# Kernel tuning notes

Hardware: AMD Instinct MI355X
Metric: run time of the kernel (lower is better)

Reference implementation:

```python
import jax, jax.numpy as jnp
import numpy as np

B, T, DIM, H = 2, 2048, 2048, 16
HD = DIM // H  # 128
ROPE_BASE = 10000.0


def _rope_angles(seq_len, head_dim, offset=0, dtype=jnp.float32):
    inv_freq = 1.0 / (ROPE_BASE ** (jnp.arange(0, head_dim, 2, dtype=dtype) / head_dim))
    pos = jnp.arange(offset, offset + seq_len, dtype=dtype)
    ang = pos[:, None] * inv_freq[None, :]              # [T, HD/2]
    ang = jnp.concatenate([ang, ang], axis=-1)          # [T, HD]
    return jnp.cos(ang), jnp.sin(ang)


def _rotate_half(x):
    x1, x2 = jnp.split(x, 2, axis=-1)
    return jnp.concatenate([-x2, x1], axis=-1)


def setup_inputs() -> dict:
    key = jax.random.key(0)
    ks = jax.random.split(key, 5)
    s = 0.02
    return {
        "x": jax.random.normal(ks[0], (B, T, DIM), dtype=jnp.float32),
        "Wq": jax.random.normal(ks[1], (DIM, DIM), dtype=jnp.float32) * s,
        "Wk": jax.random.normal(ks[2], (DIM, HD), dtype=jnp.float32) * s,
        "Wv": jax.random.normal(ks[3], (DIM, HD), dtype=jnp.float32) * s,
        "Wo": jax.random.normal(ks[4], (DIM, DIM), dtype=jnp.float32) * s,
    }


def reference(x, Wq, Wk, Wv, Wo):
    # q: [B, H, T, HD]; k, v: single shared head [B, T, HD]
    q = (x @ Wq).reshape(B, T, H, HD).transpose(0, 2, 1, 3)
    k = x @ Wk
    v = x @ Wv

    # RoPE (offset=0, no kv cache)
    cos, sin = _rope_angles(T, HD, 0, x.dtype)
    q = q * cos[None, None] + _rotate_half(q) * sin[None, None]
    k = k * cos[None] + _rotate_half(k) * sin[None]

    present_k = k[:, None]  # [B, 1, T, HD]
    present_v = v[:, None]

    # MQA attention: broadcast shared KV head via einsum (no materialized expand)
    scale = 1.0 / jnp.sqrt(jnp.asarray(HD, x.dtype))
    scores = jnp.einsum('bhqd,bkd->bhqk', q, k) * scale  # [B, H, T, T]
    causal = jnp.tril(jnp.ones((T, T), dtype=bool))
    scores = jnp.where(causal[None, None], scores, jnp.finfo(scores.dtype).min)
    attn = jax.nn.softmax(scores, axis=-1)
    out = jnp.einsum('bhqk,bkd->bhqd', attn, v)          # [B, H, T, HD]
    out = out.transpose(0, 2, 1, 3).reshape(B, T, DIM) @ Wo
    return (out, present_k, present_v)
```

## Files before the change

### kernel.cpp

```cpp
#include <hip/hip_runtime.h>


typedef __attribute__((ext_vector_type(8))) short short8;
typedef __attribute__((ext_vector_type(4))) float float4v;
typedef __attribute__((ext_vector_type(4))) unsigned short ushort4v;

#define LOG2E 1.4426950408889634f
#define ATT_SCALE 0.08838834764831845f
#define RLOG 0.20762050593046014f

__device__ __forceinline__ float bf2f(ushort u) {
    union { unsigned u; float f; } v; v.u = ((unsigned)u) << 16; return v.f;
}
__device__ __forceinline__ ushort f2bf(float f) {
    union { float f; unsigned u; } v; v.f = f;
    return (ushort)((v.u + 0x7FFF + ((v.u >> 16) & 1)) >> 16);
}
__device__ __forceinline__ ushort f2bf_fast(float f) {
    union { float f; unsigned u; } v; v.f = f;
    return (ushort)((v.u + 0x8000u) >> 16);
}
__device__ __forceinline__ float4v mfma16(short8 a, short8 b, float4v c) {
    return __builtin_amdgcn_mfma_f32_16x16x32_bf16(a, b, c, 0, 0, 0);
}
__device__ __forceinline__ void gl_lds16(const ushort* g, ushort* l) {
    __builtin_amdgcn_global_load_lds(
        (const __attribute__((address_space(1))) unsigned int*)g,
        (__attribute__((address_space(3))) unsigned int*)l, 16, 0, 0);
}

__global__ __launch_bounds__(256) void prep(const float* __restrict__ x,
                                            ushort* __restrict__ x_bf,
                                            float* __restrict__ tbl) {
    int bid = blockIdx.x;
    if (bid < 512) {
        int idx = bid * 256 + threadIdx.x;
        int d = idx & 63, t = idx >> 6;
        float inv = exp2f(-(float)d * RLOG);
        float s, c;
        sincosf((float)t * inv, &s, &c);
        tbl[idx * 2] = c;  tbl[idx * 2 + 1] = s;
    } else {
        int i = ((bid - 512) * 256 + threadIdx.x) * 4;
        float4v v = *(const float4v*)&x[i];
        ushort4v u;
        #pragma unroll
        for (int r = 0; r < 4; ++r) u[r] = f2bf(v[r]);
        *(ushort4v*)&x_bf[i] = u;
    }
}

__global__ __launch_bounds__(256) void transpose_cvt(const float* __restrict__ in,
                                                     ushort* __restrict__ out,
                                                     int M, int N) {
    __shared__ ushort tile[32][33];
    int cb = blockIdx.x * 32, rb = blockIdx.y * 32;
    int x = threadIdx.x, y0 = threadIdx.y;
    #pragma unroll
    for (int i = 0; i < 32; i += 8)
        tile[y0 + i][x] = f2bf(in[(long)(rb + y0 + i) * N + cb + x]);
    __syncthreads();
    #pragma unroll
    for (int i = 0; i < 32; i += 8)
        out[(long)(cb + y0 + i) * M + rb + x] = tile[x][y0 + i];
}

__global__ __launch_bounds__(256) void transpose_bf16(const ushort* __restrict__ in,
                                                      ushort* __restrict__ out,
                                                      int M, int N) {
    __shared__ ushort tile[32][33];
    int cb = blockIdx.x * 32, rb = blockIdx.y * 32;
    int x = threadIdx.x, y0 = threadIdx.y;
    #pragma unroll
    for (int i = 0; i < 32; i += 8)
        tile[y0 + i][x] = in[(long)(rb + y0 + i) * N + cb + x];
    __syncthreads();
    #pragma unroll
    for (int i = 0; i < 32; i += 8)
        out[(long)(cb + y0 + i) * M + rb + x] = tile[x][y0 + i];
}

__global__ __launch_bounds__(256) void gemm_qkv(const ushort* __restrict__ A,
                                                const ushort* __restrict__ W,
                                                ushort* __restrict__ Cq,
                                                ushort* __restrict__ Ck,
                                                ushort* __restrict__ Cv) {
    constexpr int BM = 128, BN = 128, K = 2048;
    constexpr int SM = 64, SN = 64, MT = 4, NT = 4;
    __shared__ ushort As[BM * 32];
    __shared__ ushort Bs[BN * 32];
    const int m0 = blockIdx.y * BM, n0 = blockIdx.x * BN;
    const int tid = threadIdx.x;
    const int wave = tid >> 6, lane = tid & 63, l15 = lane & 15, quad = lane >> 4;
    const int wr = wave >> 1, wc = wave & 1;

    float4v acc[MT][NT] = {};

    for (int k0 = 0; k0 < K; k0 += 32) {
        __syncthreads();
        #pragma unroll
        for (int p = 0; p < 2; ++p) {
            int lin = (p * 4 + wave) * 64 + lane;
            int row = lin >> 2, c8 = (lin & 3) * 8;
            gl_lds16(&A[(long)(m0 + row) * K + k0 + c8], &As[(p * 4 + wave) * 512]);
        }
        #pragma unroll
        for (int p = 0; p < 2; ++p) {
            int lin = (p * 4 + wave) * 64 + lane;
            int row = lin >> 2, c8 = (lin & 3) * 8;
            gl_lds16(&W[(long)(n0 + row) * K + k0 + c8], &Bs[(p * 4 + wave) * 512]);
        }
        __syncthreads();

        short8 a[MT], b[NT];
        #pragma unroll
        for (int mt = 0; mt < MT; ++mt)
            a[mt] = *(const short8*)&As[(wr * SM + mt * 16 + l15) * 32 + quad * 8];
        #pragma unroll
        for (int nt = 0; nt < NT; ++nt)
            b[nt] = *(const short8*)&Bs[(wc * SN + nt * 16 + l15) * 32 + quad * 8];
        #pragma unroll
        for (int mt = 0; mt < MT; ++mt)
            #pragma unroll
            for (int nt = 0; nt < NT; ++nt)
                acc[mt][nt] = mfma16(a[mt], b[nt], acc[mt][nt]);
    }
    ushort* C;  int Nc, coff;
    if (n0 < 2048)      { C = Cq; Nc = 2048; coff = n0; }
    else if (n0 < 2176) { C = Ck; Nc = 128;  coff = n0 - 2048; }
    else                { C = Cv; Nc = 128;  coff = n0 - 2176; }
    #pragma unroll
    for (int mt = 0; mt < MT; ++mt)
        #pragma unroll
        for (int nt = 0; nt < NT; ++nt)
            #pragma unroll
            for (int r = 0; r < 4; ++r) {
                int row = m0 + wr * SM + mt * 16 + quad * 4 + r;
                int col = coff + wc * SN + nt * 16 + l15;
                C[(long)row * Nc + col] = f2bf(acc[mt][nt][r]);
            }
}

__global__ __launch_bounds__(256) void gemm_out(const ushort* __restrict__ A,
                                                const ushort* __restrict__ W,
                                                float* __restrict__ C) {
    constexpr int BM = 128, BN = 128, K = 2048, N = 2048;
    constexpr int SM = 64, SN = 64, MT = 4, NT = 4;
    __shared__ ushort As[BM * 32];
    __shared__ ushort Bs[BN * 32];
    const int m0 = blockIdx.y * BM, n0 = blockIdx.x * BN;
    const int tid = threadIdx.x;
    const int wave = tid >> 6, lane = tid & 63, l15 = lane & 15, quad = lane >> 4;
    const int wr = wave >> 1, wc = wave & 1;

    float4v acc[MT][NT] = {};

    for (int k0 = 0; k0 < K; k0 += 32) {
        __syncthreads();
        #pragma unroll
        for (int p = 0; p < 2; ++p) {
            int lin = (p * 4 + wave) * 64 + lane;
            int row = lin >> 2, c8 = (lin & 3) * 8;
            gl_lds16(&A[(long)(m0 + row) * K + k0 + c8], &As[(p * 4 + wave) * 512]);
        }
        #pragma unroll
        for (int p = 0; p < 2; ++p) {
            int lin = (p * 4 + wave) * 64 + lane;
            int row = lin >> 2, c8 = (lin & 3) * 8;
            gl_lds16(&W[(long)(n0 + row) * K + k0 + c8], &Bs[(p * 4 + wave) * 512]);
        }
        __syncthreads();

        short8 a[MT], b[NT];
        #pragma unroll
        for (int mt = 0; mt < MT; ++mt)
            a[mt] = *(const short8*)&As[(wr * SM + mt * 16 + l15) * 32 + quad * 8];
        #pragma unroll
        for (int nt = 0; nt < NT; ++nt)
            b[nt] = *(const short8*)&Bs[(wc * SN + nt * 16 + l15) * 32 + quad * 8];
        #pragma unroll
        for (int mt = 0; mt < MT; ++mt)
            #pragma unroll
            for (int nt = 0; nt < NT; ++nt)
                acc[mt][nt] = mfma16(a[mt], b[nt], acc[mt][nt]);
    }
    #pragma unroll
    for (int mt = 0; mt < MT; ++mt)
        #pragma unroll
        for (int nt = 0; nt < NT; ++nt)
            #pragma unroll
            for (int r = 0; r < 4; ++r) {
                int row = m0 + wr * SM + mt * 16 + quad * 4 + r;
                int col = n0 + wc * SN + nt * 16 + l15;
                C[(long)row * N + col] = acc[mt][nt][r];
            }
}

template<int BM, int BN>
__global__ __launch_bounds__(256) void gemm_bt_f32(const float* __restrict__ A32,
                                                   const ushort* __restrict__ B0,
                                                   const ushort* __restrict__ B1,
                                                   ushort* __restrict__ C0,
                                                   ushort* __restrict__ C1,
                                                   int M, int N, int K) {
    constexpr int SM = BM / 2, SN = BN / 2;
    constexpr int MT = SM / 16, NT = SN / 16;
    constexpr int LDK = 40;
    __shared__ ushort As[BM * LDK];
    __shared__ ushort Bs[BN * LDK];
    const ushort* Bm = blockIdx.z ? B1 : B0;
    ushort* C = blockIdx.z ? C1 : C0;
    const int m0 = blockIdx.y * BM, n0 = blockIdx.x * BN;
    const int tid = threadIdx.x;
    const int wave = tid >> 6, lane = tid & 63, l15 = lane & 15, quad = lane >> 4;
    const int wr = wave >> 1, wc = wave & 1;
    float4v acc[MT][NT] = {};
    for (int k0 = 0; k0 < K; k0 += 32) {
        #pragma unroll
        for (int p = 0; p < (BM * 32) / (256 * 4); ++p) {
            int lin = p * 256 + tid;
            int row = lin >> 3, c4 = (lin & 7) * 4;
            float4v v = *(const float4v*)&A32[(long)(m0 + row) * K + k0 + c4];
            ushort4v u;
            #pragma unroll
            for (int i = 0; i < 4; ++i) u[i] = f2bf(v[i]);
            *(ushort4v*)&As[row * LDK + c4] = u;
        }
        #pragma unroll
        for (int p = 0; p < (BN * 4) / 256; ++p) {
            int lin = p * 256 + tid;
            int row = lin >> 2, c8 = (lin & 3) * 8;
            *(short8*)&Bs[row * LDK + c8] =
                *(const short8*)&Bm[(long)(n0 + row) * K + k0 + c8];
        }
        __syncthreads();
        short8 a[MT], b[NT];
        #pragma unroll
        for (int mt = 0; mt < MT; ++mt)
            a[mt] = *(const short8*)&As[(wr * SM + mt * 16 + l15) * LDK + quad * 8];
        #pragma unroll
        for (int nt = 0; nt < NT; ++nt)
            b[nt] = *(const short8*)&Bs[(wc * SN + nt * 16 + l15) * LDK + quad * 8];
        #pragma unroll
        for (int mt = 0; mt < MT; ++mt)
            #pragma unroll
            for (int nt = 0; nt < NT; ++nt)
                acc[mt][nt] = mfma16(a[mt], b[nt], acc[mt][nt]);
        __syncthreads();
    }
    #pragma unroll
    for (int mt = 0; mt < MT; ++mt)
        #pragma unroll
        for (int nt = 0; nt < NT; ++nt)
            #pragma unroll
            for (int r = 0; r < 4; ++r) {
                int row = m0 + wr * SM + mt * 16 + quad * 4 + r;
                int col = n0 + wc * SN + nt * 16 + l15;
                C[(long)row * N + col] = f2bf(acc[mt][nt][r]);
            }
}

__global__ __launch_bounds__(256) void rope_k_present(ushort* __restrict__ Kw,
                                                      const ushort* __restrict__ Vw,
                                                      const float* __restrict__ tbl,
                                                      float* __restrict__ outK,
                                                      float* __restrict__ outV) {
    int idx = blockIdx.x * 256 + threadIdx.x;
    int d = idx & 63;
    int row = idx >> 6;
    int t = row & 2047;
    float c = tbl[(t * 64 + d) * 2], s = tbl[(t * 64 + d) * 2 + 1];
    long base = (long)row * 128 + d;
    float k1 = bf2f(Kw[base]), k2 = bf2f(Kw[base + 64]);
    float r1 = k1 * c - k2 * s, r2 = k2 * c + k1 * s;
    Kw[base] = f2bf(r1);  Kw[base + 64] = f2bf(r2);
    outK[base] = r1;      outK[base + 64] = r2;
    outV[base] = bf2f(Vw[base]); outV[base + 64] = bf2f(Vw[base + 64]);
}

__global__ __launch_bounds__(256, 2) void flash_mqa6(ushort* __restrict__ Q,
                                                     const ushort* __restrict__ Kg,
                                                     const ushort* __restrict__ Vt,
                                                     const float* __restrict__ tbl) {
    constexpr int T = 2048, DIM = 2048;
    constexpr float SCL2 = ATT_SCALE * LOG2E;
    constexpr int LDP = 72;
    __shared__ ushort Ks[2][64 * 128];
    __shared__ ushort Vs[2][128 * 64];
    __shared__ ushort Ps[4][16 * LDP];

    const int j = blockIdx.x;
    const int b = j >> 8, r0 = j & 255;
    const int h = r0 & 15, q4 = r0 >> 4;

    const int tid = threadIdx.x;
    const int wave = tid >> 6, lane = tid & 63, l15 = lane & 15, quad = lane >> 4;
    const int swz = l15 & 7;

    const ushort* kb_ptr = Kg + (long)b * T * 128;
    const ushort* vb_ptr = Vt + (long)b * T;

    auto stage = [&](int buf, int t) {
        const int k0 = t * 64;
        #pragma unroll
        for (int p = 0; p < 4; ++p) {
            int ci = (wave * 4 + p) * 64 + lane;
            int kr = ci >> 4, kc = ci & 15;
            gl_lds16(&kb_ptr[(long)(k0 + kr) * 128 + ((kc ^ (kr & 7)) * 8)],
                     &Ks[buf][(wave * 4 + p) * 512]);
            int vd = ci >> 3, vc = ci & 7;
            gl_lds16(&vb_ptr[(long)vd * 4096 + k0 + ((vc ^ (vd & 7)) * 8)],
                     &Vs[buf][(wave * 4 + p) * 512]);
        }
    };

    #pragma unroll 1
    for (int ht = 0; ht < 2; ++ht) {
        const int qb = ht ? (31 - q4) : q4;
        const int qbase = qb * 64;
        const int tq = qbase + wave * 16 + l15;
        const int nkb = qb + 1;

        short8 qf[4];
        const ushort* qp = Q + (long)(b * T + tq) * DIM + h * 128 + quad * 8;
        #pragma unroll
        for (int kc = 0; kc < 4; ++kc) qf[kc] = *(const short8*)(qp + kc * 32);
        #pragma unroll
        for (int kc = 0; kc < 2; ++kc) {
            float ang[16];
            const float4v* tb = (const float4v*)(tbl + ((long)tq * 64 + kc * 32 + quad * 8) * 2);
            *(float4v*)&ang[0]  = tb[0];
            *(float4v*)&ang[4]  = tb[1];
            *(float4v*)&ang[8]  = tb[2];
            *(float4v*)&ang[12] = tb[3];
            #pragma unroll
            for (int jj = 0; jj < 8; ++jj) {
                float cs = ang[2 * jj] * SCL2, sn = ang[2 * jj + 1] * SCL2;
                float x1 = bf2f((ushort)qf[kc][jj]);
                float x2 = bf2f((ushort)qf[kc + 2][jj]);
                qf[kc][jj]     = (short)f2bf(x1 * cs - x2 * sn);
                qf[kc + 2][jj] = (short)f2bf(x2 * cs + x1 * sn);
            }
        }

        float4v o[8] = {};
        float l_part = 0.f;

        stage(0, 0);
        __syncthreads();

        for (int t = 0; t < nkb; ++t) {
            const int cur = t & 1;
            if (t + 1 < nkb) stage(cur ^ 1, t + 1);

            const ushort* ksb = &Ks[cur][0];
            const ushort* vsb = &Vs[cur][0];

            float4v st[4] = {};
            #pragma unroll
            for (int sub = 0; sub < 4; ++sub) {
                const int r = sub * 16 + l15;
                #pragma unroll
                for (int kc = 0; kc < 4; ++kc) {
                    short8 kf = *(const short8*)&ksb[r * 128 + (((kc * 4 + quad) ^ swz) * 8)];
                    st[sub] = mfma16(kf, qf[kc], st[sub]);
                }
            }

            const int k0 = t * 64;
            const bool diag = (t == nkb - 1);
            ushort* Pw = &Ps[wave][0];
            #pragma unroll
            for (int sub = 0; sub < 4; ++sub) {
                ushort4v pv4;
                #pragma unroll
                for (int rr = 0; rr < 4; ++rr) {
                    float zz = st[sub][rr];
                    if (diag) {
                        int key = k0 + sub * 16 + quad * 4 + rr;
                        zz = (key <= tq) ? zz : -INFINITY;
                    }
                    float pv = exp2f(zz);
                    l_part += pv;
                    pv4[rr] = f2bf_fast(pv);
                }
                *(ushort4v*)&Pw[l15 * LDP + sub * 16 + quad * 4] = pv4;
            }

            #pragma unroll
            for (int hf = 0; hf < 2; ++hf) {
                short8 pf = *(const short8*)&Pw[l15 * LDP + hf * 32 + quad * 8];
                #pragma unroll
                for (int nt = 0; nt < 8; ++nt) {
                    short8 vf = *(const short8*)&vsb[(nt * 16 + l15) * 64 + (((hf * 4 + quad) ^ swz) * 8)];
                    o[nt] = mfma16(vf, pf, o[nt]);
                }
            }
            __syncthreads();
        }

        float rs = l_part;
        rs += __shfl_xor(rs, 16);
        rs += __shfl_xor(rs, 32);
        float inv_l = 1.0f / rs;
        ushort* dst = Q + (long)(b * T + tq) * DIM + h * 128;
        #pragma unroll
        for (int nt = 0; nt < 8; ++nt) {
            ushort4v v;
            #pragma unroll
            for (int r = 0; r < 4; ++r) v[r] = f2bf(o[nt][r] * inv_l);
            *(ushort4v*)&dst[nt * 16 + quad * 4] = v;
        }
    }
}

extern "C" void kernel_launch(void* const* d_in, const int* in_sizes, int n_in,
                              void* d_out, int out_size, void* d_ws, size_t ws_size,
                              hipStream_t stream) {
    const float* x  = (const float*)d_in[0];
    const float* Wq = (const float*)d_in[1];
    const float* Wk = (const float*)d_in[2];
    const float* Wv = (const float*)d_in[3];
    const float* Wo = (const float*)d_in[4];
    float* out = (float*)d_out;

    char* ws = (char*)d_ws;
    const bool precast = ws_size >= (46u << 20);
    dim3 tb(32, 8);

    if (precast) {
        ushort* x_bf  = (ushort*)(ws);
        ushort* q_bf  = (ushort*)(ws + (16u << 20));
        ushort* WT    = (ushort*)(ws + (32u << 20));
        ushort* k_bf  = (ushort*)(ws + (42u << 20));
        ushort* v_bf  = (ushort*)(ws + (43u << 20));
        ushort* vt_bf = (ushort*)(ws + (44u << 20));
        float*  ropet = (float*)(ws + (45u << 20));

        prep<<<8704, 256, 0, stream>>>(x, x_bf, ropet);
        transpose_cvt<<<dim3(64, 64), tb, 0, stream>>>(Wq, WT, 2048, 2048);
        transpose_cvt<<<dim3(4, 64),  tb, 0, stream>>>(Wk, WT + (long)2048 * 2048, 2048, 128);
        transpose_cvt<<<dim3(4, 64),  tb, 0, stream>>>(Wv, WT + (long)2176 * 2048, 2048, 128);

        gemm_qkv<<<dim3(18, 32), 256, 0, stream>>>(x_bf, WT, q_bf, k_bf, v_bf);

        rope_k_present<<<1024, 256, 0, stream>>>(k_bf, v_bf, ropet,
                                                 out + 8388608, out + 8912896);
        transpose_bf16<<<dim3(4, 128), tb, 0, stream>>>(v_bf, vt_bf, 4096, 128);

        flash_mqa6<<<512, 256, 0, stream>>>(q_bf, k_bf, vt_bf, ropet);

        transpose_cvt<<<dim3(64, 64), tb, 0, stream>>>(Wo, WT, 2048, 2048);
        gemm_out<<<dim3(16, 32), 256, 0, stream>>>(q_bf, WT, out);
    } else {
        ushort* q_bf  = (ushort*)(ws);
        ushort* WT    = (ushort*)(ws + (16u << 20));
        ushort* k_bf  = (ushort*)(ws + (26u << 20));
        ushort* v_bf  = (ushort*)(ws + (27u << 20));
        ushort* vt_bf = (ushort*)(ws + (28u << 20));
        float*  ropet = (float*)(ws + (29u << 20));
        ushort* WkT = WT + (long)2048 * 2048;
        ushort* WvT = WT + (long)2176 * 2048;

        prep<<<512, 256, 0, stream>>>(x, nullptr, ropet);
        transpose_cvt<<<dim3(64, 64), tb, 0, stream>>>(Wq, WT, 2048, 2048);
        transpose_cvt<<<dim3(4, 64),  tb, 0, stream>>>(Wk, WkT, 2048, 128);
        transpose_cvt<<<dim3(4, 64),  tb, 0, stream>>>(Wv, WvT, 2048, 128);

        gemm_bt_f32<128,128><<<dim3(16, 32, 1), 256, 0, stream>>>(
            x, WT, WT, q_bf, q_bf, 4096, 2048, 2048);
        gemm_bt_f32<64,64><<<dim3(2, 64, 2), 256, 0, stream>>>(
            x, WkT, WvT, k_bf, v_bf, 4096, 128, 2048);

        rope_k_present<<<1024, 256, 0, stream>>>(k_bf, v_bf, ropet,
                                                 out + 8388608, out + 8912896);
        transpose_bf16<<<dim3(4, 128), tb, 0, stream>>>(v_bf, vt_bf, 4096, 128);

        flash_mqa6<<<512, 256, 0, stream>>>(q_bf, k_bf, vt_bf, ropet);

        transpose_cvt<<<dim3(64, 64), tb, 0, stream>>>(Wo, WT, 2048, 2048);
        gemm_out<<<dim3(16, 32), 256, 0, stream>>>(q_bf, WT, out);
    }
}
```

Measured before the change: 299.3 us.

## Restructure flash MQA to one query tile per block with 32-key tiles

```diff
diff --git a/kernel.cpp b/kernel.cpp
--- a/kernel.cpp
+++ b/kernel.cpp
@@ -278,139 +278,137 @@
     outV[base] = bf2f(Vw[base]); outV[base + 64] = bf2f(Vw[base + 64]);
 }
 
-__global__ __launch_bounds__(256, 2) void flash_mqa6(ushort* __restrict__ Q,
+__global__ __launch_bounds__(256, 4) void flash_mqa8(ushort* __restrict__ Q,
                                                      const ushort* __restrict__ Kg,
                                                      const ushort* __restrict__ Vt,
                                                      const float* __restrict__ tbl) {
     constexpr int T = 2048, DIM = 2048;
     constexpr float SCL2 = ATT_SCALE * LOG2E;
-    constexpr int LDP = 72;
-    __shared__ ushort Ks[2][64 * 128];
-    __shared__ ushort Vs[2][128 * 64];
+    constexpr int LDP = 40;
+    __shared__ ushort Ks[2][32 * 128];
+    __shared__ ushort Vs[2][128 * 32];
     __shared__ ushort Ps[4][16 * LDP];
 
-    const int j = blockIdx.x;
-    const int b = j >> 8, r0 = j & 255;
-    const int h = r0 & 15, q4 = r0 >> 4;
+    const int i = blockIdx.x;
+    const int j = i >> 5, bh = i & 31;
+    const int qb = (j < 16) ? (31 - j) : (j - 16);
+    const int b = bh >> 4, h = bh & 15;
+    const int qbase = qb * 64;
 
     const int tid = threadIdx.x;
     const int wave = tid >> 6, lane = tid & 63, l15 = lane & 15, quad = lane >> 4;
     const int swz = l15 & 7;
+    const int tq = qbase + wave * 16 + l15;
+    const int qminw = qbase + wave * 16;
+    const int nkb = 2 * qb + 2;
 
     const ushort* kb_ptr = Kg + (long)b * T * 128;
     const ushort* vb_ptr = Vt + (long)b * T;
 
+    short8 qf[4];
+    const ushort* qp = Q + (long)(b * T + tq) * DIM + h * 128 + quad * 8;
+    #pragma unroll
+    for (int kc = 0; kc < 4; ++kc) qf[kc] = *(const short8*)(qp + kc * 32);
+    #pragma unroll
+    for (int kc = 0; kc < 2; ++kc) {
+        float ang[16];
+        const float4v* tb = (const float4v*)(tbl + ((long)tq * 64 + kc * 32 + quad * 8) * 2);
+        *(float4v*)&ang[0]  = tb[0];
+        *(float4v*)&ang[4]  = tb[1];
+        *(float4v*)&ang[8]  = tb[2];
+        *(float4v*)&ang[12] = tb[3];
+        #pragma unroll
+        for (int jj = 0; jj < 8; ++jj) {
+            float cs = ang[2 * jj] * SCL2, sn = ang[2 * jj + 1] * SCL2;
+            float x1 = bf2f((ushort)qf[kc][jj]);
+            float x2 = bf2f((ushort)qf[kc + 2][jj]);
+            qf[kc][jj]     = (short)f2bf(x1 * cs - x2 * sn);
+            qf[kc + 2][jj] = (short)f2bf(x2 * cs + x1 * sn);
+        }
+    }
+
+    float4v o[8] = {};
+    float l_part = 0.f;
+
     auto stage = [&](int buf, int t) {
-        const int k0 = t * 64;
-        #pragma unroll
-        for (int p = 0; p < 4; ++p) {
-            int ci = (wave * 4 + p) * 64 + lane;
+        const int k0 = t * 32;
+        #pragma unroll
+        for (int p = 0; p < 2; ++p) {
+            int ci = (wave * 2 + p) * 64 + lane;
             int kr = ci >> 4, kc = ci & 15;
             gl_lds16(&kb_ptr[(long)(k0 + kr) * 128 + ((kc ^ (kr & 7)) * 8)],
-                     &Ks[buf][(wave * 4 + p) * 512]);
-            int vd = ci >> 3, vc = ci & 7;
-            gl_lds16(&vb_ptr[(long)vd * 4096 + k0 + ((vc ^ (vd & 7)) * 8)],
-                     &Vs[buf][(wave * 4 + p) * 512]);
+                     &Ks[buf][(wave * 2 + p) * 512]);
+            int vd = ci >> 2, vc = ci & 3;
+            gl_lds16(&vb_ptr[(long)vd * 4096 + k0 + ((vc ^ (vd & 3)) * 8)],
+                     &Vs[buf][(wave * 2 + p) * 512]);
         }
     };
 
-    #pragma unroll 1
-    for (int ht = 0; ht < 2; ++ht) {
-        const int qb = ht ? (31 - q4) : q4;
-        const int qbase = qb * 64;
-        const int tq = qbase + wave * 16 + l15;
-        const int nkb = qb + 1;
-
-        short8 qf[4];
-        const ushort* qp = Q + (long)(b * T + tq) * DIM + h * 128 + quad * 8;
-        #pragma unroll
-        for (int kc = 0; kc < 4; ++kc) qf[kc] = *(const short8*)(qp + kc * 32);
-        #pragma unroll
-        for (int kc = 0; kc < 2; ++kc) {
-            float ang[16];
-            const float4v* tb = (const float4v*)(tbl + ((long)tq * 64 + kc * 32 + quad * 8) * 2);
-            *(float4v*)&ang[0]  = tb[0];
-            *(float4v*)&ang[4]  = tb[1];
-            *(float4v*)&ang[8]  = tb[2];
-            *(float4v*)&ang[12] = tb[3];
-            #pragma unroll
-            for (int jj = 0; jj < 8; ++jj) {
-                float cs = ang[2 * jj] * SCL2, sn = ang[2 * jj + 1] * SCL2;
-                float x1 = bf2f((ushort)qf[kc][jj]);
-                float x2 = bf2f((ushort)qf[kc + 2][jj]);
-                qf[kc][jj]     = (short)f2bf(x1 * cs - x2 * sn);
-                qf[kc + 2][jj] = (short)f2bf(x2 * cs + x1 * sn);
+    stage(0, 0);
+    __syncthreads();
+
+    for (int t = 0; t < nkb; ++t) {
+        const int cur = t & 1;
+        if (t + 1 < nkb) stage(cur ^ 1, t + 1);
+
+        const ushort* ksb = &Ks[cur][0];
+        const ushort* vsb = &Vs[cur][0];
+
+        float4v st[2] = {};
+        __builtin_amdgcn_s_setprio(1);
+        #pragma unroll
+        for (int sub = 0; sub < 2; ++sub) {
+            const int r = sub * 16 + l15;
+            #pragma unroll
+            for (int kc = 0; kc < 4; ++kc) {
+                short8 kf = *(const short8*)&ksb[r * 128 + (((kc * 4 + quad) ^ swz) * 8)];
+                st[sub] = mfma16(kf, qf[kc], st[sub]);
             }
         }
-
-        float4v o[8] = {};
-        float l_part = 0.f;
-
-        stage(0, 0);
-        __syncthreads();
-
-        for (int t = 0; t < nkb; ++t) {
-            const int cur = t & 1;
-            if (t + 1 < nkb) stage(cur ^ 1, t + 1);
-
-            const ushort* ksb = &Ks[cur][0];
-            const ushort* vsb = &Vs[cur][0];
-
-            float4v st[4] = {};
-            #pragma unroll
-            for (int sub = 0; sub < 4; ++sub) {
-                const int r = sub * 16 + l15;
-                #pragma unroll
-                for (int kc = 0; kc < 4; ++kc) {
-                    short8 kf = *(const short8*)&ksb[r * 128 + (((kc * 4 + quad) ^ swz) * 8)];
-                    st[sub] = mfma16(kf, qf[kc], st[sub]);
+        __builtin_amdgcn_s_setprio(0);
+
+        const int k0 = t * 32;
+        const bool diag = (k0 + 31 > qminw);
+        ushort* Pw = &Ps[wave][0];
+        #pragma unroll
+        for (int sub = 0; sub < 2; ++sub) {
+            ushort4v pv4;
+            #pragma unroll
+            for (int rr = 0; rr < 4; ++rr) {
+                float zz = st[sub][rr];
+                if (diag) {
+                    int key = k0 + sub * 16 + quad * 4 + rr;
+                    zz = (key <= tq) ? zz : -INFINITY;
                 }
+                float pv = exp2f(zz);
+                l_part += pv;
+                pv4[rr] = f2bf_fast(pv);
             }
-
-            const int k0 = t * 64;
-            const bool diag = (t == nkb - 1);
-            ushort* Pw = &Ps[wave][0];
-            #pragma unroll
-            for (int sub = 0; sub < 4; ++sub) {
-                ushort4v pv4;
-                #pragma unroll
-                for (int rr = 0; rr < 4; ++rr) {
-                    float zz = st[sub][rr];
-                    if (diag) {
-                        int key = k0 + sub * 16 + quad * 4 + rr;
-                        zz = (key <= tq) ? zz : -INFINITY;
-                    }
-                    float pv = exp2f(zz);
-                    l_part += pv;
-                    pv4[rr] = f2bf_fast(pv);
-                }
-                *(ushort4v*)&Pw[l15 * LDP + sub * 16 + quad * 4] = pv4;
-            }
-
-            #pragma unroll
-            for (int hf = 0; hf < 2; ++hf) {
-                short8 pf = *(const short8*)&Pw[l15 * LDP + hf * 32 + quad * 8];
-                #pragma unroll
-                for (int nt = 0; nt < 8; ++nt) {
-                    short8 vf = *(const short8*)&vsb[(nt * 16 + l15) * 64 + (((hf * 4 + quad) ^ swz) * 8)];
-                    o[nt] = mfma16(vf, pf, o[nt]);
-                }
-            }
-            __syncthreads();
-        }
-
-        float rs = l_part;
-        rs += __shfl_xor(rs, 16);
-        rs += __shfl_xor(rs, 32);
-        float inv_l = 1.0f / rs;
-        ushort* dst = Q + (long)(b * T + tq) * DIM + h * 128;
+            *(ushort4v*)&Pw[l15 * LDP + sub * 16 + quad * 4] = pv4;
+        }
+
+        short8 pf = *(const short8*)&Pw[l15 * LDP + quad * 8];
+        __builtin_amdgcn_s_setprio(1);
         #pragma unroll
         for (int nt = 0; nt < 8; ++nt) {
-            ushort4v v;
-            #pragma unroll
-            for (int r = 0; r < 4; ++r) v[r] = f2bf(o[nt][r] * inv_l);
-            *(ushort4v*)&dst[nt * 16 + quad * 4] = v;
-        }
+            short8 vf = *(const short8*)&vsb[(nt * 16 + l15) * 32 + ((quad ^ (l15 & 3)) * 8)];
+            o[nt] = mfma16(vf, pf, o[nt]);
+        }
+        __builtin_amdgcn_s_setprio(0);
+        __syncthreads();
+    }
+
+    float rs = l_part;
+    rs += __shfl_xor(rs, 16);
+    rs += __shfl_xor(rs, 32);
+    float inv_l = 1.0f / rs;
+    ushort* dst = Q + (long)(b * T + tq) * DIM + h * 128;
+    #pragma unroll
+    for (int nt = 0; nt < 8; ++nt) {
+        ushort4v v;
+        #pragma unroll
+        for (int r = 0; r < 4; ++r) v[r] = f2bf(o[nt][r] * inv_l);
+        *(ushort4v*)&dst[nt * 16 + quad * 4] = v;
     }
 }
 
@@ -448,7 +446,7 @@
                                                  out + 8388608, out + 8912896);
         transpose_bf16<<<dim3(4, 128), tb, 0, stream>>>(v_bf, vt_bf, 4096, 128);
 
-        flash_mqa6<<<512, 256, 0, stream>>>(q_bf, k_bf, vt_bf, ropet);
+        flash_mqa8<<<1024, 256, 0, stream>>>(q_bf, k_bf, vt_bf, ropet);
 
         transpose_cvt<<<dim3(64, 64), tb, 0, stream>>>(Wo, WT, 2048, 2048);
         gemm_out<<<dim3(16, 32), 256, 0, stream>>>(q_bf, WT, out);
@@ -476,7 +474,7 @@
                                                  out + 8388608, out + 8912896);
         transpose_bf16<<<dim3(4, 128), tb, 0, stream>>>(v_bf, vt_bf, 4096, 128);
 
-        flash_mqa6<<<512, 256, 0, stream>>>(q_bf, k_bf, vt_bf, ropet);
+        flash_mqa8<<<1024, 256, 0, stream>>>(q_bf, k_bf, vt_bf, ropet);
 
         transpose_cvt<<<dim3(64, 64), tb, 0, stream>>>(Wo, WT, 2048, 2048);
         gemm_out<<<dim3(16, 32), 256, 0, stream>>>(q_bf, WT, out);
```

After: 306.4 us. 2.3% more time.

## Process 128-query tiles per block with two query groups per wave sharing K/V

Applied to the files above, without the earlier changes.

```diff
diff --git a/kernel.cpp b/kernel.cpp
--- a/kernel.cpp
+++ b/kernel.cpp
@@ -278,7 +278,7 @@
     outV[base] = bf2f(Vw[base]); outV[base + 64] = bf2f(Vw[base + 64]);
 }
 
-__global__ __launch_bounds__(256, 2) void flash_mqa6(ushort* __restrict__ Q,
+__global__ __launch_bounds__(256, 2) void flash_mqa9(ushort* __restrict__ Q,
                                                      const ushort* __restrict__ Kg,
                                                      const ushort* __restrict__ Vt,
                                                      const float* __restrict__ tbl) {
@@ -289,16 +289,53 @@
     __shared__ ushort Vs[2][128 * 64];
     __shared__ ushort Ps[4][16 * LDP];
 
-    const int j = blockIdx.x;
-    const int b = j >> 8, r0 = j & 255;
-    const int h = r0 & 15, q4 = r0 >> 4;
+    const int i = blockIdx.x;
+    int bh, qb;
+    if (i < 256) { bh = i >> 3;         qb = 15 - (i & 7); }
+    else         { bh = (i - 256) >> 3; qb = i & 7; }
+    const int b = bh >> 4, h = bh & 15;
+    const int qbase = qb * 128;
 
     const int tid = threadIdx.x;
     const int wave = tid >> 6, lane = tid & 63, l15 = lane & 15, quad = lane >> 4;
     const int swz = l15 & 7;
+    const int qminw = qbase + wave * 32;
+    const int nkb = 2 * qb + 2;
 
     const ushort* kb_ptr = Kg + (long)b * T * 128;
     const ushort* vb_ptr = Vt + (long)b * T;
+
+    int tq[2];
+    tq[0] = qminw + l15;
+    tq[1] = qminw + 16 + l15;
+
+    short8 qf[2][4];
+    #pragma unroll
+    for (int qg = 0; qg < 2; ++qg) {
+        const ushort* qp = Q + (long)(b * T + tq[qg]) * DIM + h * 128 + quad * 8;
+        #pragma unroll
+        for (int kc = 0; kc < 4; ++kc) qf[qg][kc] = *(const short8*)(qp + kc * 32);
+        #pragma unroll
+        for (int kc = 0; kc < 2; ++kc) {
+            float ang[16];
+            const float4v* tb = (const float4v*)(tbl + ((long)tq[qg] * 64 + kc * 32 + quad * 8) * 2);
+            *(float4v*)&ang[0]  = tb[0];
+            *(float4v*)&ang[4]  = tb[1];
+            *(float4v*)&ang[8]  = tb[2];
+            *(float4v*)&ang[12] = tb[3];
+            #pragma unroll
+            for (int jj = 0; jj < 8; ++jj) {
+                float cs = ang[2 * jj] * SCL2, sn = ang[2 * jj + 1] * SCL2;
+                float x1 = bf2f((ushort)qf[qg][kc][jj]);
+                float x2 = bf2f((ushort)qf[qg][kc + 2][jj]);
+                qf[qg][kc][jj]     = (short)f2bf(x1 * cs - x2 * sn);
+                qf[qg][kc + 2][jj] = (short)f2bf(x2 * cs + x1 * sn);
+            }
+        }
+    }
+
+    float4v o[2][8] = {};
+    float l_part[2] = {0.f, 0.f};
 
     auto stage = [&](int buf, int t) {
         const int k0 = t * 64;
@@ -314,62 +351,34 @@
         }
     };
 
-    #pragma unroll 1
-    for (int ht = 0; ht < 2; ++ht) {
-        const int qb = ht ? (31 - q4) : q4;
-        const int qbase = qb * 64;
-        const int tq = qbase + wave * 16 + l15;
-        const int nkb = qb + 1;
-
-        short8 qf[4];
-        const ushort* qp = Q + (long)(b * T + tq) * DIM + h * 128 + quad * 8;
-        #pragma unroll
-        for (int kc = 0; kc < 4; ++kc) qf[kc] = *(const short8*)(qp + kc * 32);
-        #pragma unroll
-        for (int kc = 0; kc < 2; ++kc) {
-            float ang[16];
-            const float4v* tb = (const float4v*)(tbl + ((long)tq * 64 + kc * 32 + quad * 8) * 2);
-            *(float4v*)&ang[0]  = tb[0];
-            *(float4v*)&ang[4]  = tb[1];
-            *(float4v*)&ang[8]  = tb[2];
-            *(float4v*)&ang[12] = tb[3];
-            #pragma unroll
-            for (int jj = 0; jj < 8; ++jj) {
-                float cs = ang[2 * jj] * SCL2, sn = ang[2 * jj + 1] * SCL2;
-                float x1 = bf2f((ushort)qf[kc][jj]);
-                float x2 = bf2f((ushort)qf[kc + 2][jj]);
-                qf[kc][jj]     = (short)f2bf(x1 * cs - x2 * sn);
-                qf[kc + 2][jj] = (short)f2bf(x2 * cs + x1 * sn);
-            }
-        }
-
-        float4v o[8] = {};
-        float l_part = 0.f;
-
-        stage(0, 0);
-        __syncthreads();
-
-        for (int t = 0; t < nkb; ++t) {
-            const int cur = t & 1;
-            if (t + 1 < nkb) stage(cur ^ 1, t + 1);
-
-            const ushort* ksb = &Ks[cur][0];
-            const ushort* vsb = &Vs[cur][0];
-
+    stage(0, 0);
+    __syncthreads();
+
+    for (int t = 0; t < nkb; ++t) {
+        const int cur = t & 1;
+        if (t + 1 < nkb) stage(cur ^ 1, t + 1);
+
+        const ushort* ksb = &Ks[cur][0];
+        const ushort* vsb = &Vs[cur][0];
+        const int k0 = t * 64;
+        const bool diag = (k0 + 63 > qminw);
+        ushort* Pw = &Ps[wave][0];
+
+        #pragma unroll
+        for (int qg = 0; qg < 2; ++qg) {
             float4v st[4] = {};
+            __builtin_amdgcn_s_setprio(1);
             #pragma unroll
             for (int sub = 0; sub < 4; ++sub) {
                 const int r = sub * 16 + l15;
                 #pragma unroll
                 for (int kc = 0; kc < 4; ++kc) {
                     short8 kf = *(const short8*)&ksb[r * 128 + (((kc * 4 + quad) ^ swz) * 8)];
-                    st[sub] = mfma16(kf, qf[kc], st[sub]);
+                    st[sub] = mfma16(kf, qf[qg][kc], st[sub]);
                 }
             }
-
-            const int k0 = t * 64;
-            const bool diag = (t == nkb - 1);
-            ushort* Pw = &Ps[wave][0];
+            __builtin_amdgcn_s_setprio(0);
+
             #pragma unroll
             for (int sub = 0; sub < 4; ++sub) {
                 ushort4v pv4;
@@ -378,37 +387,42 @@
                     float zz = st[sub][rr];
                     if (diag) {
                         int key = k0 + sub * 16 + quad * 4 + rr;
-                        zz = (key <= tq) ? zz : -INFINITY;
+                        zz = (key <= tq[qg]) ? zz : -INFINITY;
                     }
                     float pv = exp2f(zz);
-                    l_part += pv;
+                    l_part[qg] += pv;
                     pv4[rr] = f2bf_fast(pv);
                 }
                 *(ushort4v*)&Pw[l15 * LDP + sub * 16 + quad * 4] = pv4;
             }
 
+            __builtin_amdgcn_s_setprio(1);
             #pragma unroll
             for (int hf = 0; hf < 2; ++hf) {
                 short8 pf = *(const short8*)&Pw[l15 * LDP + hf * 32 + quad * 8];
                 #pragma unroll
                 for (int nt = 0; nt < 8; ++nt) {
                     short8 vf = *(const short8*)&vsb[(nt * 16 + l15) * 64 + (((hf * 4 + quad) ^ swz) * 8)];
-                    o[nt] = mfma16(vf, pf, o[nt]);
+                    o[qg][nt] = mfma16(vf, pf, o[qg][nt]);
                 }
             }
-            __syncthreads();
-        }
-
-        float rs = l_part;
+            __builtin_amdgcn_s_setprio(0);
+        }
+        __syncthreads();
+    }
+
+    #pragma unroll
+    for (int qg = 0; qg < 2; ++qg) {
+        float rs = l_part[qg];
         rs += __shfl_xor(rs, 16);
         rs += __shfl_xor(rs, 32);
         float inv_l = 1.0f / rs;
-        ushort* dst = Q + (long)(b * T + tq) * DIM + h * 128;
+        ushort* dst = Q + (long)(b * T + tq[qg]) * DIM + h * 128;
         #pragma unroll
         for (int nt = 0; nt < 8; ++nt) {
             ushort4v v;
             #pragma unroll
-            for (int r = 0; r < 4; ++r) v[r] = f2bf(o[nt][r] * inv_l);
+            for (int r = 0; r < 4; ++r) v[r] = f2bf(o[qg][nt][r] * inv_l);
             *(ushort4v*)&dst[nt * 16 + quad * 4] = v;
         }
     }
@@ -448,7 +462,7 @@
                                                  out + 8388608, out + 8912896);
         transpose_bf16<<<dim3(4, 128), tb, 0, stream>>>(v_bf, vt_bf, 4096, 128);
 
-        flash_mqa6<<<512, 256, 0, stream>>>(q_bf, k_bf, vt_bf, ropet);
+        flash_mqa9<<<512, 256, 0, stream>>>(q_bf, k_bf, vt_bf, ropet);
 
         transpose_cvt<<<dim3(64, 64), tb, 0, stream>>>(Wo, WT, 2048, 2048);
         gemm_out<<<dim3(16, 32), 256, 0, stream>>>(q_bf, WT, out);
@@ -476,7 +490,7 @@
                                                  out + 8388608, out + 8912896);
         transpose_bf16<<<dim3(4, 128), tb, 0, stream>>>(v_bf, vt_bf, 4096, 128);
 
-        flash_mqa6<<<512, 256, 0, stream>>>(q_bf, k_bf, vt_bf, ropet);
+        flash_mqa9<<<512, 256, 0, stream>>>(q_bf, k_bf, vt_bf, ropet);
 
         transpose_cvt<<<dim3(64, 64), tb, 0, stream>>>(Wo, WT, 2048, 2048);
         gemm_out<<<dim3(16, 32), 256, 0, stream>>>(q_bf, WT, out);
```

After: 323.4 us. 8.0% more time.

## Load V fragments directly from global memory, drop V LDS staging in flash kernel

Applied to the files above, without the earlier changes.

```diff
diff --git a/kernel.cpp b/kernel.cpp
--- a/kernel.cpp
+++ b/kernel.cpp
@@ -278,15 +278,14 @@
     outV[base] = bf2f(Vw[base]); outV[base + 64] = bf2f(Vw[base + 64]);
 }
 
-__global__ __launch_bounds__(256, 2) void flash_mqa6(ushort* __restrict__ Q,
-                                                     const ushort* __restrict__ Kg,
-                                                     const ushort* __restrict__ Vt,
-                                                     const float* __restrict__ tbl) {
+__global__ __launch_bounds__(256, 3) void flash_mqa10(ushort* __restrict__ Q,
+                                                      const ushort* __restrict__ Kg,
+                                                      const ushort* __restrict__ Vt,
+                                                      const float* __restrict__ tbl) {
     constexpr int T = 2048, DIM = 2048;
     constexpr float SCL2 = ATT_SCALE * LOG2E;
     constexpr int LDP = 72;
     __shared__ ushort Ks[2][64 * 128];
-    __shared__ ushort Vs[2][128 * 64];
     __shared__ ushort Ps[4][16 * LDP];
 
     const int j = blockIdx.x;
@@ -308,9 +307,6 @@
             int kr = ci >> 4, kc = ci & 15;
             gl_lds16(&kb_ptr[(long)(k0 + kr) * 128 + ((kc ^ (kr & 7)) * 8)],
                      &Ks[buf][(wave * 4 + p) * 512]);
-            int vd = ci >> 3, vc = ci & 7;
-            gl_lds16(&vb_ptr[(long)vd * 4096 + k0 + ((vc ^ (vd & 7)) * 8)],
-                     &Vs[buf][(wave * 4 + p) * 512]);
         }
     };
 
@@ -354,9 +350,10 @@
             if (t + 1 < nkb) stage(cur ^ 1, t + 1);
 
             const ushort* ksb = &Ks[cur][0];
-            const ushort* vsb = &Vs[cur][0];
+            const int k0 = t * 64;
 
             float4v st[4] = {};
+            __builtin_amdgcn_s_setprio(1);
             #pragma unroll
             for (int sub = 0; sub < 4; ++sub) {
                 const int r = sub * 16 + l15;
@@ -366,9 +363,18 @@
                     st[sub] = mfma16(kf, qf[kc], st[sub]);
                 }
             }
-
-            const int k0 = t * 64;
-            const bool diag = (t == nkb - 1);
+            __builtin_amdgcn_s_setprio(0);
+
+            short8 vf0[8], vf1[8];
+            #pragma unroll
+            for (int nt = 0; nt < 8; ++nt)
+                vf0[nt] = *(const short8*)&vb_ptr[(long)(nt * 16 + l15) * 4096 + k0 + quad * 8];
+            #pragma unroll
+            for (int nt = 0; nt < 8; ++nt)
+                vf1[nt] = *(const short8*)&vb_ptr[(long)(nt * 16 + l15) * 4096 + k0 + 32 + quad * 8];
+
+            const int qminw = qbase + wave * 16;
+            const bool diag = (k0 + 63 > qminw);
             ushort* Pw = &Ps[wave][0];
             #pragma unroll
             for (int sub = 0; sub < 4; ++sub) {
@@ -387,15 +393,15 @@
                 *(ushort4v*)&Pw[l15 * LDP + sub * 16 + quad * 4] = pv4;
             }
 
-            #pragma unroll
-            for (int hf = 0; hf < 2; ++hf) {
-                short8 pf = *(const short8*)&Pw[l15 * LDP + hf * 32 + quad * 8];
-                #pragma unroll
-                for (int nt = 0; nt < 8; ++nt) {
-                    short8 vf = *(const short8*)&vsb[(nt * 16 + l15) * 64 + (((hf * 4 + quad) ^ swz) * 8)];
-                    o[nt] = mfma16(vf, pf, o[nt]);
-                }
-            }
+            short8 pf0 = *(const short8*)&Pw[l15 * LDP + quad * 8];
+            short8 pf1 = *(const short8*)&Pw[l15 * LDP + 32 + quad * 8];
+            __builtin_amdgcn_s_setprio(1);
+            #pragma unroll
+            for (int nt = 0; nt < 8; ++nt) o[nt] = mfma16(vf0[nt], pf0, o[nt]);
+            #pragma unroll
+            for (int nt = 0; nt < 8; ++nt) o[nt] = mfma16(vf1[nt], pf1, o[nt]);
+            __builtin_amdgcn_s_setprio(0);
+
             __syncthreads();
         }
 
@@ -448,7 +454,7 @@
                                                  out + 8388608, out + 8912896);
         transpose_bf16<<<dim3(4, 128), tb, 0, stream>>>(v_bf, vt_bf, 4096, 128);
 
-        flash_mqa6<<<512, 256, 0, stream>>>(q_bf, k_bf, vt_bf, ropet);
+        flash_mqa10<<<512, 256, 0, stream>>>(q_bf, k_bf, vt_bf, ropet);
 
         transpose_cvt<<<dim3(64, 64), tb, 0, stream>>>(Wo, WT, 2048, 2048);
         gemm_out<<<dim3(16, 32), 256, 0, stream>>>(q_bf, WT, out);
@@ -476,7 +482,7 @@
                                                  out + 8388608, out + 8912896);
         transpose_bf16<<<dim3(4, 128), tb, 0, stream>>>(v_bf, vt_bf, 4096, 128);
 
-        flash_mqa6<<<512, 256, 0, stream>>>(q_bf, k_bf, vt_bf, ropet);
+        flash_mqa10<<<512, 256, 0, stream>>>(q_bf, k_bf, vt_bf, ropet);
 
         transpose_cvt<<<dim3(64, 64), tb, 0, stream>>>(Wo, WT, 2048, 2048);
         gemm_out<<<dim3(16, 32), 256, 0, stream>>>(q_bf, WT, out);
```

New measurement: 386.3 us. 1.29x slower.
